# Optimization experiments

Measured on AMD Instinct MI355X. Metric: run time of the kernel, lower is better.

Reference implementation:

```python
import jax, jax.numpy as jnp
import numpy as np

# Dimensions inferred from the module (few-shot reweighted YOLOv2 region loss)
B, C, NA, NCPA = 64, 20, 5, 1          # batch, base classes, anchors, classes-per-anchor
H, W = 19, 19                           # feature map (608 input / stride 32)
T = 50                                  # cfg.max_boxes
THRESH = 0.6
COORD_SCALE = 1.0
CLASS_SCALE = 1.0
NB = B * C                              # per-class 'image' rows, as in the torch code
A4 = NA * H * W
EPS = 1e-12
BCE_EPS = 1e-7
ANCHORS = [[1.3221, 1.73145], [3.19275, 4.00944], [5.05587, 8.09892], [9.47112, 4.84053], [11.2364, 10.0071]]


def iou_xywh(x1, y1, w1, h1, x2, y2, w2, h2):
    # center-size IoU, matches darknet bbox_iou(x1y1x2y2=False)
    l = jnp.maximum(x1 - w1 * 0.5, x2 - w2 * 0.5)
    r = jnp.minimum(x1 + w1 * 0.5, x2 + w2 * 0.5)
    t = jnp.maximum(y1 - h1 * 0.5, y2 - h2 * 0.5)
    b = jnp.minimum(y1 + h1 * 0.5, y2 + h2 * 0.5)
    inter = jnp.clip(r - l, 0.0) * jnp.clip(b - t, 0.0)
    union = w1 * h1 + w2 * h2 - inter
    return inter / jnp.maximum(union, EPS)


def setup_inputs() -> dict:
    key = jax.random.key(0)
    k1, k2, k3, k4 = jax.random.split(key, 4)
    output = jax.random.normal(k1, (NB, NA * (5 + NCPA), H, W), jnp.float32) * 0.5
    # target rows: [cls, x, y, w, h] * T, coords in (0,1); x kept > 0 so all boxes are 'valid'
    cls_ids = jax.random.randint(k2, (B, C, T), 0, C).astype(jnp.float32)
    xy = jax.random.uniform(k3, (B, C, T, 2), minval=0.05, maxval=0.95)
    wh = jax.random.uniform(k4, (B, C, T, 2), minval=0.05, maxval=0.5)
    target = jnp.concatenate([cls_ids[..., None], xy, wh], axis=-1).reshape(B, C, T * 5)
    anchors = jnp.asarray(ANCHORS, jnp.float32)
    return {"output": output, "target": target, "anchors": anchors}


def _forward(output, target, anchors):
    target = jax.lax.stop_gradient(target)
    anchors = jax.lax.stop_gradient(anchors)
    out5 = output.reshape(NB, NA, 5 + NCPA, H, W)
    x = jax.nn.sigmoid(out5[:, :, 0])
    y = jax.nn.sigmoid(out5[:, :, 1])
    w = out5[:, :, 2]
    h = out5[:, :, 3]
    conf = jax.nn.sigmoid(out5[:, :, 4])
    # class logits regrouped to original batch: (B*NA*H*W, C)
    cls = out5[:, :, 5:5 + NCPA].reshape(NB, NA, H, W)
    cls_logits = cls.reshape(B, C, NA * H * W).transpose(0, 2, 1).reshape(-1, C)
    # decode pred boxes (detached, mirroring torch's use of .data)
    grid_x = jnp.arange(W, dtype=jnp.float32)[None, None, None, :]
    grid_y = jnp.arange(H, dtype=jnp.float32)[None, None, :, None]
    aw = anchors[:, 0][None, :, None, None]
    ah = anchors[:, 1][None, :, None, None]
    px = jax.lax.stop_gradient(x) + grid_x
    py = jax.lax.stop_gradient(y) + grid_y
    pw = jnp.exp(jax.lax.stop_gradient(w)) * aw
    ph = jnp.exp(jax.lax.stop_gradient(h)) * ah
    # ground-truth boxes per row
    tgt = target.reshape(NB, T, 5)
    cls_t = tgt[:, :, 0]
    gx = tgt[:, :, 1] * W
    gy = tgt[:, :, 2] * H
    gw = tgt[:, :, 3] * W
    gh = tgt[:, :, 4] * H
    # 'break on first zero x' semantics
    valid = jnp.cumprod((tgt[:, :, 1] != 0).astype(jnp.int32), axis=1) > 0
    # stage 1: zero conf_mask where any gt IoU > thresh (scan over T to avoid (NB,T,A4) blowup)
    pxf = px.reshape(NB, A4); pyf = py.reshape(NB, A4)
    pwf = pw.reshape(NB, A4); phf = ph.reshape(NB, A4)

    def iou_step(ci, xs):
        gxt, gyt, gwt, ght, vt = xs
        iou = iou_xywh(pxf, pyf, pwf, phf, gxt[:, None], gyt[:, None], gwt[:, None], ght[:, None])
        return jnp.maximum(ci, jnp.where(vt[:, None], iou, 0.0)), None

    cur_ious, _ = jax.lax.scan(iou_step, jnp.zeros((NB, A4), jnp.float32), (gx.T, gy.T, gw.T, gh.T, valid.T))
    conf_mask0 = jnp.where(cur_ious.reshape(NB, NA, H, W) > THRESH, 0.0, 1.0)
    # best anchor per gt by wh-only IoU
    inter = jnp.minimum(gw[..., None], anchors[:, 0]) * jnp.minimum(gh[..., None], anchors[:, 1])
    union = gw[..., None] * gh[..., None] + anchors[:, 0] * anchors[:, 1] - inter
    best_n = jnp.argmax(inter / jnp.maximum(union, EPS), axis=-1).astype(jnp.int32)  # (NB,T)
    gi = gx.astype(jnp.int32)
    gj = gy.astype(jnp.int32)
    # stage 2: ordered scatter of targets (later boxes overwrite earlier, as in the torch loops)
    binds = jnp.arange(NB)
    z = jnp.zeros((NB, NA, H, W), jnp.float32)
    # seen < 12800 branch: tx=ty=0.5, tw=th=0, coord_mask=1
    carry0 = (jnp.ones_like(z), z, conf_mask0, jnp.full_like(z, 0.5), jnp.full_like(z, 0.5), z, z, z, z)

    def tgt_step(carry, xs):
        cm, clm, cfm, tx, ty, tw, th, tconf, tcls = carry
        gxt, gyt, gwt, ght, bn, git, gjt, vt, ct = xs
        idx = (binds, bn, gjt, git)

        def upd(arr, val):
            return arr.at[idx].set(jnp.where(vt, val, arr[idx]))

        aw_b = anchors[bn, 0]
        ah_b = anchors[bn, 1]
        iou = iou_xywh(gxt, gyt, gwt, ght, px[idx], py[idx], pw[idx], ph[idx])
        cm = upd(cm, 1.0)
        clm = upd(clm, 1.0)
        cfm = upd(cfm, 1.0)
        tx = upd(tx, gxt - git.astype(jnp.float32))
        ty = upd(ty, gyt - gjt.astype(jnp.float32))
        tw = upd(tw, jnp.log(jnp.maximum(gwt, EPS) / aw_b))
        th = upd(th, jnp.log(jnp.maximum(ght, EPS) / ah_b))
        tconf = upd(tconf, iou)
        tcls = upd(tcls, ct)
        return (cm, clm, cfm, tx, ty, tw, th, tconf, tcls), None

    xs = (gx.T, gy.T, gw.T, gh.T, best_n.T, gi.T, gj.T, valid.T, cls_t.T)
    (coord_mask, cls_mask, conf_mask, tx, ty, tw, th, tconf, tcls), _ = jax.lax.scan(tgt_step, carry0, xs)
    # regroup per-class rows back to original batch (neg_ratio='full' -> counts[i] == C)
    cm_grp = cls_mask.reshape(B, C, NA, H, W).sum(axis=1)
    tcls_grp = tcls.reshape(B, C, NA, H, W).sum(axis=1)
    sel = (cm_grp == 1.0).reshape(-1)           # exclude colliding cells
    labels = tcls_grp.reshape(-1).astype(jnp.int32)

    def bce_mean(p, t):
        p = jnp.clip(p, BCE_EPS, 1.0 - BCE_EPS)
        return jnp.mean(-(t * jnp.log(p) + (1.0 - t) * jnp.log(1.0 - p)))

    loss_x = COORD_SCALE * bce_mean(x * coord_mask, tx * coord_mask)
    loss_y = COORD_SCALE * bce_mean(y * coord_mask, ty * coord_mask)
    loss_w = COORD_SCALE * 0.5 * jnp.mean((w * coord_mask - tw * coord_mask) ** 2)
    loss_h = COORD_SCALE * 0.5 * jnp.mean((h * coord_mask - th * coord_mask) ** 2)
    loss_conf = 0.5 * jnp.mean((conf * conf_mask - tconf * conf_mask) ** 2)
    logp = jax.nn.log_softmax(cls_logits, axis=-1)
    nll = -jnp.take_along_axis(logp, labels[:, None], axis=1)[:, 0]
    nsel = jnp.maximum(jnp.sum(sel.astype(jnp.float32)), 1.0)
    loss_cls = CLASS_SCALE * jnp.sum(jnp.where(sel, nll, 0.0)) / nsel
    return loss_x + loss_y + loss_w + loss_h + loss_conf + loss_cls


def reference(output, target, anchors):
    return _forward(output, target, anchors)
```

## Files before the change

kernel.cpp:

```cpp
#include <hip/hip_runtime.h>
#include <math.h>

constexpr int cB   = 64;
constexpr int cC   = 20;
constexpr int cNA  = 5;
constexpr int cH   = 19;
constexpr int cW   = 19;
constexpr int cT   = 50;
constexpr int cNB  = cB * cC;
constexpr int cHW  = cH * cW;
constexpr int cA4  = cNA * cHW;
constexpr int cCH  = cNA * 6;
constexpr long cNTOT = (long)cNB * cA4;
constexpr int cCLS_BLOCKS = cB * cNA * 2;

__device__ __constant__ float cAW[cNA]   = {1.3221f, 3.19275f, 5.05587f, 9.47112f, 11.2364f};
__device__ __constant__ float cAH[cNA]   = {1.73145f, 4.00944f, 8.09892f, 4.84053f, 10.0071f};
__device__ __constant__ float cAREA[cNA] = {2.28930345f, 12.80114796f, 40.94706183f, 45.84455262f, 112.44377644f};
__device__ __constant__ float cLNAW[cNA] = {0.27920469f, 1.16088088f, 1.62060702f, 2.24822684f, 2.41915174f};
__device__ __constant__ float cLNAH[cNA] = {0.54896100f, 1.38865236f, 2.09173157f, 1.57701337f, 2.30329495f};

constexpr int ACC_BANKS = 64;
constexpr size_t OFF_CNT  = 2560;
constexpr size_t OFF_ROW  = 4096;
constexpr size_t ZERO_BYTES = OFF_ROW + (size_t)cB * cA4 * 4;
constexpr size_t OFF_SBOX = ZERO_BYTES;

__device__ __forceinline__ float fexp(float x) {
    return __builtin_amdgcn_exp2f(x * 1.4426950408889634f);
}
__device__ __forceinline__ float flog(float x) {
    return __builtin_amdgcn_logf(x) * 0.6931471805599453f;
}
__device__ __forceinline__ float frcp(float x) { return __builtin_amdgcn_rcpf(x); }
__device__ __forceinline__ float fsigmoid(float x) { return frcp(1.0f + fexp(-x)); }

typedef _Float16 h2 __attribute__((ext_vector_type(2)));
union HU { unsigned u; h2 h; };
__device__ __forceinline__ unsigned splat2(float v) {
    HU x; _Float16 f = (_Float16)v; x.h[0] = f; x.h[1] = f; return x.u;
}
constexpr float cS = 1.2649110640673518f;

__global__ void k_prep_box(const float* __restrict__ target, unsigned* __restrict__ sbox) {
    const int nb = blockIdx.x;
    const int t  = threadIdx.x;
    float xr = 1.f, yr = 0.f, wr = 0.f, hr = 0.f;
    if (t < cT) {
        const float* tg = target + (size_t)nb * (cT * 5) + t * 5;
        xr = tg[1]; yr = tg[2]; wr = tg[3]; hr = tg[4];
    }
    unsigned long long nz = __ballot(xr != 0.0f);
    if (t < cT) {
        unsigned long long below = (2ull << t) - 1ull;
        bool valid = ((~nz) & below) == 0ull;
        uint4 w0, w1;
        if (valid) {
            float gx = xr * (float)cW, gy = yr * (float)cH;
            float gw = wr * (float)cW, gh = hr * (float)cH;
            w0 = make_uint4(splat2(cS * (gx - 0.5f * gw)),
                            splat2(cS * (gx + 0.5f * gw)),
                            splat2(cS * (gy - 0.5f * gh)),
                            splat2(cS * (gy + 0.5f * gh)));
            w1 = make_uint4(splat2(-0.6f * (gw * gh)), 0u, 0u, 0u);
        } else {
            w0 = make_uint4(splat2(1e4f), splat2(-1e4f), splat2(1e4f), splat2(-1e4f));
            w1 = make_uint4(splat2(0.0f), 0u, 0u, 0u);
        }
        uint4* dst = (uint4*)(sbox + (size_t)nb * 400 + t * 8);
        dst[0] = w0;
        dst[1] = w1;
    }
}

__launch_bounds__(256)
__global__ void k_main(const float* __restrict__ outp, const float* __restrict__ target,
                       const unsigned* __restrict__ sbox,
                       int* __restrict__ rowenc, double* __restrict__ acc) {
    __shared__ int s_win[cA4];
    __shared__ int s_tc[cT];
    __shared__ __align__(16) float4 s_gt[cT];
    __shared__ double s_red[3][4];
    const int tid  = threadIdx.x;
    const int nb   = blockIdx.x >> 1;
    const int half = blockIdx.x & 1;
    const int base = (half << 10) + tid;
    const int b_   = nb / cC;
    const int c_   = nb - b_ * cC;
    const float* obase = outp + (size_t)nb * (cCH * cHW);

    for (int k = tid; k < cA4; k += 256) s_win[k] = -1;
    __syncthreads();

    if (tid < 64) {
        const int t = tid;
        float xr = 1.f, yr = 0.f, wr = 0.f, hr = 0.f;
        if (t < cT) {
            const float* tg = target + (size_t)nb * (cT * 5) + t * 5;
            xr = tg[1]; yr = tg[2]; wr = tg[3]; hr = tg[4];
        }
        unsigned long long nz = __ballot(xr != 0.0f);
        if (t < cT) {
            unsigned long long below = (2ull << t) - 1ull;
            bool valid = ((~nz) & below) == 0ull;
            float gx = xr * (float)cW, gy = yr * (float)cH;
            float gw = wr * (float)cW, gh = hr * (float)cH;
            s_gt[t] = make_float4(gx, gy, gw, gh);
            if (valid) {
                float garea = gw * gh;
                float best = -1.0f; int bn = 0;
                for (int n = 0; n < cNA; ++n) {
                    float inter = fminf(gw, cAW[n]) * fminf(gh, cAH[n]);
                    float uni   = garea + cAREA[n] - inter;
                    float r = inter / fmaxf(uni, 1e-12f);
                    if (r > best) { best = r; bn = n; }
                }
                int cell = bn * cHW + (int)gy * cW + (int)gx;
                s_tc[t] = cell;
                atomicMax(&s_win[cell], t);
            } else {
                s_tc[t] = -1;
            }
        }
    }
    __syncthreads();
    if (half == 0 && tid < cT) {
        int cell = s_tc[tid];
        if (cell >= 0 && s_win[cell] == tid)
            atomicAdd(&rowenc[b_ * cA4 + cell], (1 << 10) | (c_ * cT + tid));
    }

    h2 pl2[2], pr2[2], pt2[2], pb2[2], ov2[2], pa06h[2];
    float conf[4], tcf[4];
    unsigned wbits = 0;
    float bce = 0.0f, sq = 0.0f;
    const h2 z2 = { (_Float16)0.0f, (_Float16)0.0f };

    #pragma unroll
    for (int u = 0; u < 4; ++u) {
        int cell = base + (u << 8);
        bool a_  = cell < cA4;
        int cc   = a_ ? cell : (cA4 - 1);
        int na   = cc / cHW;
        int rem  = cc - na * cHW;
        int j    = rem / cW;
        int i    = rem - j * cW;
        const float* ob = obase + (size_t)(na * 6) * cHW + rem;
        float xl = ob[0], yl = ob[cHW], wl = ob[2*cHW], hl = ob[3*cHW], cl = ob[4*cHW];
        float aw = cAW[na], ah = cAH[na];
        float x  = fsigmoid(xl), y = fsigmoid(yl), cf = fsigmoid(cl);
        float px = x + (float)i, py = y + (float)j;
        float pw = fexp(wl) * aw, ph = fexp(hl) * ah;
        float l0 = px - 0.5f*pw, r0 = px + 0.5f*pw;
        float t0 = py - 0.5f*ph, b0 = py + 0.5f*ph;
        float pa = pw * ph;
        int p = u >> 1, s = u & 1;
        if (a_) {
            pl2[p][s] = (_Float16)(cS * l0);  pr2[p][s] = (_Float16)(cS * r0);
            pt2[p][s] = (_Float16)(cS * t0);  pb2[p][s] = (_Float16)(cS * b0);
        } else {
            pl2[p][s] = (_Float16)1e4f;  pr2[p][s] = (_Float16)(-1e4f);
            pt2[p][s] = (_Float16)1e4f;  pb2[p][s] = (_Float16)(-1e4f);
        }
        pa06h[p][s] = (_Float16)(0.6f * pa);
        ov2[p][s] = (_Float16)0.0f;
        conf[u] = cf; tcf[u] = 0.0f;

        float tx = 0.5f, ty = 0.5f, tw = 0.0f, th = 0.0f;
        int wt = s_win[cc];
        bool wfl = (wt >= 0) && a_;
        if (wfl) {
            wbits |= (1u << u);
            float4 g = s_gt[wt];
            float gx = g.x, gy = g.y, gw = g.z, gh = g.w;
            tx = gx - (float)i; ty = gy - (float)j;
            tw = flog(fmaxf(gw, 1e-12f)) - cLNAW[na];
            th = flog(fmaxf(gh, 1e-12f)) - cLNAH[na];
            float iw = fminf(r0, gx + 0.5f*gw) - fmaxf(l0, gx - 0.5f*gw);
            float ih = fminf(b0, gy + 0.5f*gh) - fmaxf(t0, gy - 0.5f*gh);
            iw = fmaxf(iw, 0.0f); ih = fmaxf(ih, 0.0f);
            float inter = iw * ih;
            float uni   = gw*gh + pa - inter;
            tcf[u] = inter * frcp(fmaxf(uni, 1e-12f));
        }
        if (a_) {
            float pc = fminf(fmaxf(x, 1e-7f), 1.0f - 1e-7f);
            bce += -(tx * flog(pc) + (1.0f - tx) * flog(1.0f - pc));
            pc = fminf(fmaxf(y, 1e-7f), 1.0f - 1e-7f);
            bce += -(ty * flog(pc) + (1.0f - ty) * flog(1.0f - pc));
            float dw = wl - tw, dh = hl - th;
            sq += dw*dw + dh*dh;
        }
    }

    const unsigned* tb32 = sbox + (size_t)nb * 400;
    #pragma unroll 10
    for (int t = 0; t < cT; ++t) {
        HU a, b, c, d, e;
        a.u = tb32[t*8 + 0]; b.u = tb32[t*8 + 1];
        c.u = tb32[t*8 + 2]; d.u = tb32[t*8 + 3];
        e.u = tb32[t*8 + 4];
        #pragma unroll
        for (int p = 0; p < 2; ++p) {
            h2 iw = __builtin_elementwise_min(pr2[p], b.h) - __builtin_elementwise_max(pl2[p], a.h);
            h2 ih = __builtin_elementwise_min(pb2[p], d.h) - __builtin_elementwise_max(pt2[p], c.h);
            iw = __builtin_elementwise_max(iw, z2);
            ih = __builtin_elementwise_max(ih, z2);
            ov2[p] = __builtin_elementwise_max(ov2[p], iw * ih + e.h);
        }
    }

    float sc = 0.0f;
    #pragma unroll
    for (int u = 0; u < 4; ++u) {
        int cell = base + (u << 8);
        if (cell >= cA4) continue;
        int p = u >> 1, s = u & 1;
        bool wfl  = (wbits >> u) & 1;
        bool over = ov2[p][s] > pa06h[p][s];
        float cm  = wfl ? 1.0f : (over ? 0.0f : 1.0f);
        float d   = (conf[u] - tcf[u]) * cm;
        sc += d * d;
    }

    double v0 = (double)bce, v1 = (double)sq, v2 = (double)sc;
    for (int off = 32; off > 0; off >>= 1) {
        v0 += __shfl_down(v0, off);
        v1 += __shfl_down(v1, off);
        v2 += __shfl_down(v2, off);
    }
    int lane = tid & 63, wid = tid >> 6;
    if (lane == 0) { s_red[0][wid] = v0; s_red[1][wid] = v1; s_red[2][wid] = v2; }
    __syncthreads();
    if (tid == 0) {
        double a0 = s_red[0][0] + s_red[0][1] + s_red[0][2] + s_red[0][3];
        double a1 = s_red[1][0] + s_red[1][1] + s_red[1][2] + s_red[1][3];
        double a2 = s_red[2][0] + s_red[2][1] + s_red[2][2] + s_red[2][3];
        int bank = blockIdx.x & (ACC_BANKS - 1);
        atomicAdd(&acc[0*ACC_BANKS + bank], a0);
        atomicAdd(&acc[1*ACC_BANKS + bank], a1);
        atomicAdd(&acc[2*ACC_BANKS + bank], a2);
    }
}

__launch_bounds__(192)
__global__ void k_cls(const float* __restrict__ outp, const float* __restrict__ target,
                      const int* __restrict__ rowenc, double* __restrict__ acc,
                      int* __restrict__ cnt, float* __restrict__ out) {
    __shared__ double s_red[2][3];
    __shared__ int s_last;
    const int tid  = threadIdx.x;
    const int blk  = blockIdx.x;
    const int b    = blk / (cNA * 2);
    const int r2   = blk - b * (cNA * 2);
    const int na   = r2 >> 1;
    const int half = r2 & 1;
    const int rem  = half * 192 + tid;
    double nll = 0.0, ns = 0.0;
    if (rem < cHW) {
        const float* ob = outp + ((size_t)(b * cC) * cCH + na * 6 + 5) * cHW + rem;
        float l[cC]; float m = -1e30f;
        #pragma unroll
        for (int c = 0; c < cC; ++c) {
            l[c] = ob[(size_t)c * (cCH * cHW)];
            m = fmaxf(m, l[c]);
        }
        float s = 0.0f;
        #pragma unroll
        for (int c = 0; c < cC; ++c) s += fexp(l[c] - m);
        float lse = m + flog(s);
        int v = rowenc[b * cA4 + na * cHW + rem];
        if ((v >> 10) == 1) {
            int payload = v & 1023;
            int selc = payload / cT;
            int selt = payload - selc * cT;
            int label = (int)target[((size_t)(b * cC + selc) * cT + selt) * 5];
            nll = (double)(lse - l[label]);
            ns  = 1.0;
        }
    }
    for (int off = 32; off > 0; off >>= 1) {
        nll += __shfl_down(nll, off);
        ns  += __shfl_down(ns, off);
    }
    int lane = tid & 63, wid = tid >> 6;
    if (lane == 0) { s_red[0][wid] = nll; s_red[1][wid] = ns; }
    __syncthreads();
    if (tid == 0) {
        double a0 = s_red[0][0] + s_red[0][1] + s_red[0][2];
        double a1 = s_red[1][0] + s_red[1][1] + s_red[1][2];
        int bank = blk & (ACC_BANKS - 1);
        atomicAdd(&acc[3*ACC_BANKS + bank], a0);
        atomicAdd(&acc[4*ACC_BANKS + bank], a1);
        __threadfence();
        s_last = (atomicAdd(cnt, 1) == cCLS_BLOCKS - 1);
    }
    __syncthreads();
    if (s_last && tid < 64) {
        __threadfence();
        double s[5];
        #pragma unroll
        for (int j = 0; j < 5; ++j) {
            double v = atomicAdd(&acc[j * ACC_BANKS + tid], 0.0);
            for (int off = 32; off > 0; off >>= 1) v += __shfl_down(v, off);
            s[j] = v;
        }
        if (tid == 0) {
            double Ninv = 1.0 / (double)cNTOT;
            double loss = s[0] * Ninv
                        + 0.5 * s[1] * Ninv
                        + 0.5 * s[2] * Ninv
                        + s[3] / fmax(s[4], 1.0);
            out[0] = (float)loss;
        }
    }
}

extern "C" void kernel_launch(void* const* d_in, const int* in_sizes, int n_in,
                              void* d_out, int out_size, void* d_ws, size_t ws_size,
                              hipStream_t stream) {
    const float* output = (const float*)d_in[0];
    const float* target = (const float*)d_in[1];
    char* ws = (char*)d_ws;
    double*   acc    = (double*)ws;
    int*      cnt    = (int*)(ws + OFF_CNT);
    int*      rowenc = (int*)(ws + OFF_ROW);
    unsigned* sbox   = (unsigned*)(ws + OFF_SBOX);

    hipMemsetAsync(ws, 0, ZERO_BYTES, stream);

    k_prep_box<<<cNB, 64, 0, stream>>>(target, sbox);
    k_main<<<cNB * 2, 256, 0, stream>>>(output, target, sbox, rowenc, acc);
    k_cls<<<cCLS_BLOCKS, 192, 0, stream>>>(output, target, rowenc, acc, cnt, (float*)d_out);
}
```

Baseline: 138.3 us.

## Move target matching and winner map into prep kernel, read from global in main

The per-row target decode, best-anchor search and cell-winner resolution move from the main per-cell kernel into the small prep kernel. The prep kernel writes a full winner map and scaled GT boxes to workspace, and the cell kernel reads them from global memory instead of rebuilding them in shared memory. This removes the serial 64-thread prologue and two block barriers from each of the 2560 main blocks, and the duplicated work across the two half-blocks. In exchange it adds about 1.85 MB of winner-map writes and reads plus an extra global gather per cell.

Result: slower. 142.9 us (+3.3%).

```diff
diff --git a/kernel.cpp b/kernel.cpp
--- a/kernel.cpp
+++ b/kernel.cpp
@@ -25,6 +25,8 @@
 constexpr size_t OFF_ROW  = 4096;
 constexpr size_t ZERO_BYTES = OFF_ROW + (size_t)cB * cA4 * 4;
 constexpr size_t OFF_SBOX = ZERO_BYTES;
+constexpr size_t OFF_GT   = OFF_SBOX + 2048000;
+constexpr size_t OFF_WIN  = OFF_GT + 1024000;
 
 __device__ __forceinline__ float fexp(float x) {
     return __builtin_amdgcn_exp2f(x * 1.4426950408889634f);
@@ -42,9 +44,19 @@
 }
 constexpr float cS = 1.2649110640673518f;
 
-__global__ void k_prep_box(const float* __restrict__ target, unsigned* __restrict__ sbox) {
+__launch_bounds__(64)
+__global__ void k_prep(const float* __restrict__ target,
+                       int* __restrict__ winner, float4* __restrict__ gt4,
+                       unsigned* __restrict__ sbox, int* __restrict__ rowenc) {
+    __shared__ int s_win[cA4];
+    __shared__ int s_tc[cT];
     const int nb = blockIdx.x;
     const int t  = threadIdx.x;
+    const int b_ = nb / cC;
+    const int c_ = nb - b_ * cC;
+
+    for (int k = t; k < cA4; k += 64) s_win[k] = -1;
+
     float xr = 1.f, yr = 0.f, wr = 0.f, hr = 0.f;
     if (t < cT) {
         const float* tg = target + (size_t)nb * (cT * 5) + t * 5;
@@ -54,81 +66,55 @@
     if (t < cT) {
         unsigned long long below = (2ull << t) - 1ull;
         bool valid = ((~nz) & below) == 0ull;
+        float gx = xr * (float)cW, gy = yr * (float)cH;
+        float gw = wr * (float)cW, gh = hr * (float)cH;
+        gt4[nb * cT + t] = make_float4(gx, gy, gw, gh);
         uint4 w0, w1;
         if (valid) {
-            float gx = xr * (float)cW, gy = yr * (float)cH;
-            float gw = wr * (float)cW, gh = hr * (float)cH;
             w0 = make_uint4(splat2(cS * (gx - 0.5f * gw)),
                             splat2(cS * (gx + 0.5f * gw)),
                             splat2(cS * (gy - 0.5f * gh)),
                             splat2(cS * (gy + 0.5f * gh)));
             w1 = make_uint4(splat2(-0.6f * (gw * gh)), 0u, 0u, 0u);
+            float garea = gw * gh;
+            float best = -1.0f; int bn = 0;
+            for (int n = 0; n < cNA; ++n) {
+                float inter = fminf(gw, cAW[n]) * fminf(gh, cAH[n]);
+                float uni   = garea + cAREA[n] - inter;
+                float r = inter / fmaxf(uni, 1e-12f);
+                if (r > best) { best = r; bn = n; }
+            }
+            int cell = bn * cHW + (int)gy * cW + (int)gx;
+            s_tc[t] = cell;
+            atomicMax(&s_win[cell], t);
         } else {
             w0 = make_uint4(splat2(1e4f), splat2(-1e4f), splat2(1e4f), splat2(-1e4f));
             w1 = make_uint4(splat2(0.0f), 0u, 0u, 0u);
+            s_tc[t] = -1;
         }
         uint4* dst = (uint4*)(sbox + (size_t)nb * 400 + t * 8);
         dst[0] = w0;
         dst[1] = w1;
     }
+    __syncthreads();
+    for (int k = t; k < cA4; k += 64) winner[(size_t)nb * cA4 + k] = s_win[k];
+    if (t < cT) {
+        int cell = s_tc[t];
+        if (cell >= 0 && s_win[cell] == t)
+            atomicAdd(&rowenc[b_ * cA4 + cell], (1 << 10) | (c_ * cT + t));
+    }
 }
 
 __launch_bounds__(256)
-__global__ void k_main(const float* __restrict__ outp, const float* __restrict__ target,
-                       const unsigned* __restrict__ sbox,
-                       int* __restrict__ rowenc, double* __restrict__ acc) {
-    __shared__ int s_win[cA4];
-    __shared__ int s_tc[cT];
-    __shared__ __align__(16) float4 s_gt[cT];
+__global__ void k_cell(const float* __restrict__ outp,
+                       const int* __restrict__ winner, const float4* __restrict__ gt4,
+                       const unsigned* __restrict__ sbox, double* __restrict__ acc) {
     __shared__ double s_red[3][4];
     const int tid  = threadIdx.x;
     const int nb   = blockIdx.x >> 1;
     const int half = blockIdx.x & 1;
     const int base = (half << 10) + tid;
-    const int b_   = nb / cC;
-    const int c_   = nb - b_ * cC;
     const float* obase = outp + (size_t)nb * (cCH * cHW);
-
-    for (int k = tid; k < cA4; k += 256) s_win[k] = -1;
-    __syncthreads();
-
-    if (tid < 64) {
-        const int t = tid;
-        float xr = 1.f, yr = 0.f, wr = 0.f, hr = 0.f;
-        if (t < cT) {
-            const float* tg = target + (size_t)nb * (cT * 5) + t * 5;
-            xr = tg[1]; yr = tg[2]; wr = tg[3]; hr = tg[4];
-        }
-        unsigned long long nz = __ballot(xr != 0.0f);
-        if (t < cT) {
-            unsigned long long below = (2ull << t) - 1ull;
-            bool valid = ((~nz) & below) == 0ull;
-            float gx = xr * (float)cW, gy = yr * (float)cH;
-            float gw = wr * (float)cW, gh = hr * (float)cH;
-            s_gt[t] = make_float4(gx, gy, gw, gh);
-            if (valid) {
-                float garea = gw * gh;
-                float best = -1.0f; int bn = 0;
-                for (int n = 0; n < cNA; ++n) {
-                    float inter = fminf(gw, cAW[n]) * fminf(gh, cAH[n]);
-                    float uni   = garea + cAREA[n] - inter;
-                    float r = inter / fmaxf(uni, 1e-12f);
-                    if (r > best) { best = r; bn = n; }
-                }
-                int cell = bn * cHW + (int)gy * cW + (int)gx;
-                s_tc[t] = cell;
-                atomicMax(&s_win[cell], t);
-            } else {
-                s_tc[t] = -1;
-            }
-        }
-    }
-    __syncthreads();
-    if (half == 0 && tid < cT) {
-        int cell = s_tc[tid];
-        if (cell >= 0 && s_win[cell] == tid)
-            atomicAdd(&rowenc[b_ * cA4 + cell], (1 << 10) | (c_ * cT + tid));
-    }
 
     h2 pl2[2], pr2[2], pt2[2], pb2[2], ov2[2], pa06h[2];
     float conf[4], tcf[4];
@@ -147,6 +133,7 @@
         int i    = rem - j * cW;
         const float* ob = obase + (size_t)(na * 6) * cHW + rem;
         float xl = ob[0], yl = ob[cHW], wl = ob[2*cHW], hl = ob[3*cHW], cl = ob[4*cHW];
+        int wt = winner[(size_t)nb * cA4 + cc];
         float aw = cAW[na], ah = cAH[na];
         float x  = fsigmoid(xl), y = fsigmoid(yl), cf = fsigmoid(cl);
         float px = x + (float)i, py = y + (float)j;
@@ -167,11 +154,10 @@
         conf[u] = cf; tcf[u] = 0.0f;
 
         float tx = 0.5f, ty = 0.5f, tw = 0.0f, th = 0.0f;
-        int wt = s_win[cc];
         bool wfl = (wt >= 0) && a_;
         if (wfl) {
             wbits |= (1u << u);
-            float4 g = s_gt[wt];
+            float4 g = gt4[nb * cT + wt];
             float gx = g.x, gy = g.y, gw = g.z, gh = g.w;
             tx = gx - (float)i; ty = gy - (float)j;
             tw = flog(fmaxf(gw, 1e-12f)) - cLNAW[na];
@@ -326,10 +312,12 @@
     int*      cnt    = (int*)(ws + OFF_CNT);
     int*      rowenc = (int*)(ws + OFF_ROW);
     unsigned* sbox   = (unsigned*)(ws + OFF_SBOX);
+    float4*   gt4    = (float4*)(ws + OFF_GT);
+    int*      winner = (int*)(ws + OFF_WIN);
 
     hipMemsetAsync(ws, 0, ZERO_BYTES, stream);
 
-    k_prep_box<<<cNB, 64, 0, stream>>>(target, sbox);
-    k_main<<<cNB * 2, 256, 0, stream>>>(output, target, sbox, rowenc, acc);
+    k_prep<<<cNB, 64, 0, stream>>>(target, winner, gt4, sbox, rowenc);
+    k_cell<<<cNB * 2, 256, 0, stream>>>(output, winner, gt4, sbox, acc);
     k_cls<<<cCLS_BLOCKS, 192, 0, stream>>>(output, target, rowenc, acc, cnt, (float*)d_out);
 }
```
